# Optimization experiments

Hardware: AMD Instinct MI355X
Metric: run time of the kernel (lower is better)

## Reference

```python
import jax, jax.numpy as jnp
import numpy as np

B, K, S, H = 8, 2048, 1024, 256   # batch, num_spans, seq_len, hidden
W = 24                            # max span width (gather window)
WIN = 3
NEG_INF = -jnp.inf


def setup_inputs() -> dict:
    key = jax.random.key(0)
    k1, k2, k3, k4 = jax.random.split(key, 4)
    token_reps = jax.random.normal(k1, (B, S, H), dtype=jnp.float32)
    starts = jax.random.randint(k2, (B, K), 0, S - W)
    widths = jax.random.randint(k3, (B, K), 1, W + 1)  # span width in [1, W]
    ends = starts + widths                              # end is exclusive, <= S
    span_ids = jnp.stack([starts, ends], axis=-1).astype(jnp.int32)
    span_masks = jax.random.uniform(k4, (B, K)) < 0.9
    return {"token_reps": token_reps, "span_ids": span_ids, "span_masks": span_masks}


def _masked_max(tok_win, mask):
    # tok_win: (B, K, W, H), mask: (B, K, W) -> (B, K, H)
    return jnp.max(jnp.where(mask[..., None], tok_win, NEG_INF), axis=2)


def reference(token_reps, span_ids, span_masks):
    """extract_span_reps, mode='start_inner_maxpool_end', pooling=False.

    Equivalent math to the torch version, but gathers only the per-span window
    [start, start+W) instead of broadcasting over the full seq_len, since all
    spans have width <= W.
    """
    Bv, Sv, Hv = token_reps.shape
    starts = span_ids[..., 0]            # (B, K)
    ends = span_ids[..., 1]              # (B, K) exclusive

    pos = jnp.arange(W)                  # (W,)
    idx = starts[..., None] + pos        # (B, K, W) absolute token index
    safe_idx = jnp.clip(idx, 0, Sv - 1)  # safe gather; out-of-span masked below
    # gather per-span token windows: (B, K, W, H)
    tok_win = token_reps[jnp.arange(Bv)[:, None, None], safe_idx]

    valid = span_masks[..., None]                                 # (B, K, 1)
    start_cut = jnp.minimum(starts + WIN, ends)[..., None]        # (B, K, 1)
    end_cut = jnp.maximum(ends - WIN, starts)[..., None]          # (B, K, 1)
    e = ends[..., None]

    # idx >= start always holds (pos >= 0)
    start_m = (idx < start_cut) & valid
    end_m = (idx >= end_cut) & (idx < e) & valid
    inner_m = ((idx >= start_cut) & (idx < end_cut)
               & ((ends - starts) > 2 * WIN)[..., None] & valid)

    start_reps = _masked_max(tok_win, start_m)   # (B, K, H)
    end_reps = _masked_max(tok_win, end_m)
    inner_reps = _masked_max(tok_win, inner_m)

    # spans with no inner tokens fall back to start reps
    no_inner = jnp.isinf(inner_reps).all(axis=-1, keepdims=True)
    inner_reps = jnp.where(no_inner, start_reps, inner_reps)

    span_reps = jnp.concatenate([start_reps, inner_reps, end_reps], axis=-1)
    span_reps = jnp.where(span_masks[..., None], span_reps, 0.0)  # (B, K, 3H)
    return span_reps
```

## Files before the change

kernel.cpp:

```cpp
#include <hip/hip_runtime.h>

#define Bv   8
#define Kv   2048
#define Sv   1024
#define Hv   256
#define Wv   24
#define WINv 3
#define RB   8

#define NSPAN (Bv * Kv)

__device__ __forceinline__ float bf16_to_f32(unsigned short u) {
    union { unsigned int i; float f; } c;
    c.i = ((unsigned int)u) << 16;
    return c.f;
}

__global__ __launch_bounds__(256) void span_rep_kernel(
    const void* __restrict__ token_reps,
    const int* __restrict__ span_ids,
    const void* __restrict__ span_masks,
    float* __restrict__ out)
{
    __shared__ int s_tok32;
    __shared__ int s_ids64;
    __shared__ int s_maskw;

    const int tid = threadIdx.x;
    if (tid < 64) {
        const unsigned short* tu = (const unsigned short*)token_reps;
        int e = (tu[2 * tid] >> 7) & 0xFF;
        unsigned long long votes = __ballot(e >= 96 && e <= 144);

        const unsigned char* mb = (const unsigned char*)span_masks;
        unsigned char bnz = mb[tid] | mb[tid + 64];
        int m4 = tid & 3;
        unsigned long long z1  = __ballot(bnz && m4 == 1);
        unsigned long long z23 = __ballot(bnz && (m4 == 2 || m4 == 3));
        unsigned long long z84 = __ballot(bnz && m4 == 0 && (tid & 7) == 4);

        if (tid == 0) {
            s_tok32 = (__popcll(votes) >= 56) ? 0 : 1;
            s_maskw = z1 ? 0 : (z23 ? 3 : (z84 ? 1 : 2));
            int odd_or = span_ids[1] | span_ids[3] | span_ids[5] | span_ids[7];
            s_ids64 = (odd_or == 0) ? 1 : 0;
        }
    }
    __syncthreads();

    const int span = blockIdx.x * 4 + (tid >> 6);
    const int lane = tid & 63;

    float4* out4 = (float4*)(out + (size_t)span * (3 * Hv)) + lane;

    int mv;
    if (s_maskw == 0)      mv = ((const unsigned char*)span_masks)[span];
    else if (s_maskw == 1) mv = ((const int*)span_masks)[span];
    else if (s_maskw == 2) mv = ((const int*)span_masks)[2 * span];
    else                   mv = (((const float*)span_masks)[span] != 0.0f);

    int start, end;
    if (!s_ids64) {
        start = span_ids[2 * span];
        end   = span_ids[2 * span + 1];
    } else {
        start = span_ids[4 * span];
        end   = span_ids[4 * span + 2];
    }
    const int w = end - start;

    if (mv == 0 || w < 1 || w > Wv || start < 0 || end > Sv) {
        float4 z = make_float4(0.f, 0.f, 0.f, 0.f);
        out4[0]       = z;
        out4[Hv / 4]  = z;
        out4[Hv / 2]  = z;
        return;
    }

    const int b = span >> 11;
    const size_t row0 = ((size_t)b * Sv + start) * Hv;

    float s0 = -INFINITY, s1 = -INFINITY, s2 = -INFINITY, s3 = -INFINITY;
    float e0 = -INFINITY, e1 = -INFINITY, e2 = -INFINITY, e3 = -INFINITY;
    float i0 = -INFINITY, i1 = -INFINITY, i2 = -INFINITY, i3 = -INFINITY;

    const int  scut      = (w < WINv) ? w : WINv;
    const int  ecut      = (w - WINv > 0) ? (w - WINv) : 0;
    const bool has_inner = (w > 2 * WINv);
    const int  icut      = w - WINv;

    if (s_tok32) {
        const float4* tp = (const float4*)((const float*)token_reps + row0) + lane;
        for (int r0 = 0; r0 < w; r0 += RB) {
            const int n = ((w - r0) < RB) ? (w - r0) : RB;
            float4 buf[RB];
            #pragma unroll
            for (int j = 0; j < RB; ++j)
                if (j < n) buf[j] = tp[(size_t)(r0 + j) * (Hv / 4)];
            #pragma unroll
            for (int j = 0; j < RB; ++j) {
                if (j < n) {
                    const int r = r0 + j;
                    float4 f = buf[j];
                    if (r < scut) {
                        s0 = fmaxf(s0, f.x); s1 = fmaxf(s1, f.y);
                        s2 = fmaxf(s2, f.z); s3 = fmaxf(s3, f.w);
                    }
                    if (r >= ecut) {
                        e0 = fmaxf(e0, f.x); e1 = fmaxf(e1, f.y);
                        e2 = fmaxf(e2, f.z); e3 = fmaxf(e3, f.w);
                    }
                    if (has_inner && r >= WINv && r < icut) {
                        i0 = fmaxf(i0, f.x); i1 = fmaxf(i1, f.y);
                        i2 = fmaxf(i2, f.z); i3 = fmaxf(i3, f.w);
                    }
                }
            }
        }
    } else {
        const unsigned short* tp = (const unsigned short*)token_reps + row0 + lane * 4;
        for (int r0 = 0; r0 < w; r0 += RB) {
            const int n = ((w - r0) < RB) ? (w - r0) : RB;
            ushort4 buf[RB];
            #pragma unroll
            for (int j = 0; j < RB; ++j)
                if (j < n) buf[j] = *(const ushort4*)(tp + (size_t)(r0 + j) * Hv);
            #pragma unroll
            for (int j = 0; j < RB; ++j) {
                if (j < n) {
                    const int r = r0 + j;
                    float f0 = bf16_to_f32(buf[j].x), f1 = bf16_to_f32(buf[j].y);
                    float f2 = bf16_to_f32(buf[j].z), f3 = bf16_to_f32(buf[j].w);
                    if (r < scut) {
                        s0 = fmaxf(s0, f0); s1 = fmaxf(s1, f1);
                        s2 = fmaxf(s2, f2); s3 = fmaxf(s3, f3);
                    }
                    if (r >= ecut) {
                        e0 = fmaxf(e0, f0); e1 = fmaxf(e1, f1);
                        e2 = fmaxf(e2, f2); e3 = fmaxf(e3, f3);
                    }
                    if (has_inner && r >= WINv && r < icut) {
                        i0 = fmaxf(i0, f0); i1 = fmaxf(i1, f1);
                        i2 = fmaxf(i2, f2); i3 = fmaxf(i3, f3);
                    }
                }
            }
        }
    }
    if (!has_inner) { i0 = s0; i1 = s1; i2 = s2; i3 = s3; }

    out4[0]      = make_float4(s0, s1, s2, s3);
    out4[Hv / 4] = make_float4(i0, i1, i2, i3);
    out4[Hv / 2] = make_float4(e0, e1, e2, e3);
}

extern "C" void kernel_launch(void* const* d_in, const int* in_sizes, int n_in,
                              void* d_out, int out_size, void* d_ws, size_t ws_size,
                              hipStream_t stream) {
    const void* token_reps = d_in[0];
    const int*  span_ids   = (const int*)d_in[1];
    const void* span_masks = d_in[2];
    for (int i = 0; i < n_in; ++i) {
        if (in_sizes[i] == Bv * Sv * Hv)      token_reps = d_in[i];
        else if (in_sizes[i] == Bv * Kv * 2)  span_ids   = (const int*)d_in[i];
        else if (in_sizes[i] == Bv * Kv)      span_masks = d_in[i];
    }
    float* out = (float*)d_out;

    dim3 grid(NSPAN / 4);
    dim3 block(256);
    span_rep_kernel<<<grid, block, 0, stream>>>(token_reps, span_ids, span_masks, out);
}
```

Baseline: 91.00 us.

## Process eight spans per wave, drop shared-memory format probe, use nontemporal stores

Each wavefront now handles eight consecutive spans instead of one, and the grid shrinks to match. Blocks are interleaved across batches, so concurrently running blocks read from different batch rows. The per-block input-format detection moves from a shared-memory write followed by a barrier to per-wave ballots, which removes the __syncthreads. Outputs are written with nontemporal stores so they do not pollute the cache. In exchange, far fewer waves are in flight to hide gather latency, and every wave repeats the format probe loads.

Result: slower. 97.44 us (+7.1%).

```diff
diff --git a/kernel.cpp b/kernel.cpp
--- a/kernel.cpp
+++ b/kernel.cpp
@@ -7,13 +7,21 @@
 #define Wv   24
 #define WINv 3
 #define RB   8
+#define SPW  8
 
 #define NSPAN (Bv * Kv)
+
+typedef float nt4 __attribute__((ext_vector_type(4)));
 
 __device__ __forceinline__ float bf16_to_f32(unsigned short u) {
     union { unsigned int i; float f; } c;
     c.i = ((unsigned int)u) << 16;
     return c.f;
+}
+
+__device__ __forceinline__ void nt_store4(float* p, float a, float b, float c, float d) {
+    nt4 v = {a, b, c, d};
+    __builtin_nontemporal_store(v, (nt4*)p);
 }
 
 __global__ __launch_bounds__(256) void span_rep_kernel(
@@ -22,136 +30,123 @@
     const void* __restrict__ span_masks,
     float* __restrict__ out)
 {
-    __shared__ int s_tok32;
-    __shared__ int s_ids64;
-    __shared__ int s_maskw;
-
-    const int tid = threadIdx.x;
-    if (tid < 64) {
-        const unsigned short* tu = (const unsigned short*)token_reps;
-        int e = (tu[2 * tid] >> 7) & 0xFF;
-        unsigned long long votes = __ballot(e >= 96 && e <= 144);
-
-        const unsigned char* mb = (const unsigned char*)span_masks;
-        unsigned char bnz = mb[tid] | mb[tid + 64];
-        int m4 = tid & 3;
-        unsigned long long z1  = __ballot(bnz && m4 == 1);
-        unsigned long long z23 = __ballot(bnz && (m4 == 2 || m4 == 3));
-        unsigned long long z84 = __ballot(bnz && m4 == 0 && (tid & 7) == 4);
-
-        if (tid == 0) {
-            s_tok32 = (__popcll(votes) >= 56) ? 0 : 1;
-            s_maskw = z1 ? 0 : (z23 ? 3 : (z84 ? 1 : 2));
-            int odd_or = span_ids[1] | span_ids[3] | span_ids[5] | span_ids[7];
-            s_ids64 = (odd_or == 0) ? 1 : 0;
-        }
-    }
-    __syncthreads();
-
-    const int span = blockIdx.x * 4 + (tid >> 6);
+    const int tid  = threadIdx.x;
     const int lane = tid & 63;
 
-    float4* out4 = (float4*)(out + (size_t)span * (3 * Hv)) + lane;
+    const unsigned short* tu = (const unsigned short*)token_reps;
+    int e = (tu[2 * lane] >> 7) & 0xFF;
+    unsigned long long votes = __ballot(e >= 96 && e <= 144);
+    const int tok32 = (__popcll(votes) >= 56) ? 0 : 1;
 
-    int mv;
-    if (s_maskw == 0)      mv = ((const unsigned char*)span_masks)[span];
-    else if (s_maskw == 1) mv = ((const int*)span_masks)[span];
-    else if (s_maskw == 2) mv = ((const int*)span_masks)[2 * span];
-    else                   mv = (((const float*)span_masks)[span] != 0.0f);
+    const unsigned char* mbp = (const unsigned char*)span_masks;
+    unsigned char bnz = mbp[lane] | mbp[lane + 64];
+    int m4 = lane & 3;
+    unsigned long long z1  = __ballot(bnz && m4 == 1);
+    unsigned long long z23 = __ballot(bnz && (m4 == 2 || m4 == 3));
+    unsigned long long z84 = __ballot(bnz && m4 == 0 && (lane & 7) == 4);
+    const int maskw = z1 ? 0 : (z23 ? 3 : (z84 ? 1 : 2));
 
-    int start, end;
-    if (!s_ids64) {
-        start = span_ids[2 * span];
-        end   = span_ids[2 * span + 1];
-    } else {
-        start = span_ids[4 * span];
-        end   = span_ids[4 * span + 2];
-    }
-    const int w = end - start;
+    const int odd_or = span_ids[1] | span_ids[3] | span_ids[5] | span_ids[7];
+    const int ids64 = (odd_or == 0) ? 1 : 0;
 
-    if (mv == 0 || w < 1 || w > Wv || start < 0 || end > Sv) {
-        float4 z = make_float4(0.f, 0.f, 0.f, 0.f);
-        out4[0]       = z;
-        out4[Hv / 4]  = z;
-        out4[Hv / 2]  = z;
-        return;
+    const int b     = blockIdx.x & 7;
+    const int kbase = ((blockIdx.x >> 3) << 5) + ((tid >> 6) << 3);
+    const int span0 = b * Kv + kbase;
+
+    int st[SPW], en[SPW], mvv[SPW];
+    #pragma unroll
+    for (int j = 0; j < SPW; ++j) {
+        const int span = span0 + j;
+        if (!ids64) {
+            st[j] = span_ids[2 * span];
+            en[j] = span_ids[2 * span + 1];
+        } else {
+            st[j] = span_ids[4 * span];
+            en[j] = span_ids[4 * span + 2];
+        }
+        if (maskw == 0)      mvv[j] = ((const unsigned char*)span_masks)[span];
+        else if (maskw == 1) mvv[j] = ((const int*)span_masks)[span];
+        else if (maskw == 2) mvv[j] = ((const int*)span_masks)[2 * span];
+        else                 mvv[j] = (((const float*)span_masks)[span] != 0.0f);
     }
 
-    const int b = span >> 11;
-    const size_t row0 = ((size_t)b * Sv + start) * Hv;
+    const size_t batch_off = (size_t)b * Sv * Hv;
 
-    float s0 = -INFINITY, s1 = -INFINITY, s2 = -INFINITY, s3 = -INFINITY;
-    float e0 = -INFINITY, e1 = -INFINITY, e2 = -INFINITY, e3 = -INFINITY;
-    float i0 = -INFINITY, i1 = -INFINITY, i2 = -INFINITY, i3 = -INFINITY;
+    for (int j = 0; j < SPW; ++j) {
+        const int span = span0 + j;
+        float* outp = out + (size_t)span * (3 * Hv) + lane * 4;
 
-    const int  scut      = (w < WINv) ? w : WINv;
-    const int  ecut      = (w - WINv > 0) ? (w - WINv) : 0;
-    const bool has_inner = (w > 2 * WINv);
-    const int  icut      = w - WINv;
+        const int start = st[j];
+        const int w     = en[j] - start;
 
-    if (s_tok32) {
-        const float4* tp = (const float4*)((const float*)token_reps + row0) + lane;
-        for (int r0 = 0; r0 < w; r0 += RB) {
-            const int n = ((w - r0) < RB) ? (w - r0) : RB;
-            float4 buf[RB];
-            #pragma unroll
-            for (int j = 0; j < RB; ++j)
-                if (j < n) buf[j] = tp[(size_t)(r0 + j) * (Hv / 4)];
-            #pragma unroll
-            for (int j = 0; j < RB; ++j) {
-                if (j < n) {
-                    const int r = r0 + j;
-                    float4 f = buf[j];
-                    if (r < scut) {
-                        s0 = fmaxf(s0, f.x); s1 = fmaxf(s1, f.y);
-                        s2 = fmaxf(s2, f.z); s3 = fmaxf(s3, f.w);
-                    }
-                    if (r >= ecut) {
-                        e0 = fmaxf(e0, f.x); e1 = fmaxf(e1, f.y);
-                        e2 = fmaxf(e2, f.z); e3 = fmaxf(e3, f.w);
-                    }
-                    if (has_inner && r >= WINv && r < icut) {
-                        i0 = fmaxf(i0, f.x); i1 = fmaxf(i1, f.y);
-                        i2 = fmaxf(i2, f.z); i3 = fmaxf(i3, f.w);
-                    }
-                }
+        if (mvv[j] == 0 || w < 1 || w > Wv || start < 0 || en[j] > Sv) {
+            nt_store4(outp,          0.f, 0.f, 0.f, 0.f);
+            nt_store4(outp + Hv,     0.f, 0.f, 0.f, 0.f);
+            nt_store4(outp + 2 * Hv, 0.f, 0.f, 0.f, 0.f);
+            continue;
+        }
+
+        const size_t row0 = batch_off + (size_t)start * Hv;
+
+        float s0 = -INFINITY, s1 = -INFINITY, s2 = -INFINITY, s3 = -INFINITY;
+        float e0 = -INFINITY, e1 = -INFINITY, e2 = -INFINITY, e3 = -INFINITY;
+        float i0 = -INFINITY, i1 = -INFINITY, i2 = -INFINITY, i3 = -INFINITY;
+
+        const int  scut      = (w < WINv) ? w : WINv;
+        const int  ecut      = (w - WINv > 0) ? (w - WINv) : 0;
+        const bool has_inner = (w > 2 * WINv);
+        const int  icut      = w - WINv;
+
+        auto reduce = [&](int r, float f0, float f1, float f2, float f3) {
+            if (r < scut) {
+                s0 = fmaxf(s0, f0); s1 = fmaxf(s1, f1);
+                s2 = fmaxf(s2, f2); s3 = fmaxf(s3, f3);
+            }
+            if (r >= ecut) {
+                e0 = fmaxf(e0, f0); e1 = fmaxf(e1, f1);
+                e2 = fmaxf(e2, f2); e3 = fmaxf(e3, f3);
+            }
+            if (has_inner && r >= WINv && r < icut) {
+                i0 = fmaxf(i0, f0); i1 = fmaxf(i1, f1);
+                i2 = fmaxf(i2, f2); i3 = fmaxf(i3, f3);
+            }
+        };
+
+        if (tok32) {
+            const float4* tp = (const float4*)((const float*)token_reps + row0) + lane;
+            for (int r0 = 0; r0 < w; r0 += RB) {
+                const int n = ((w - r0) < RB) ? (w - r0) : RB;
+                float4 buf[RB];
+                #pragma unroll
+                for (int jj = 0; jj < RB; ++jj)
+                    if (jj < n) buf[jj] = tp[(size_t)(r0 + jj) * (Hv / 4)];
+                #pragma unroll
+                for (int jj = 0; jj < RB; ++jj)
+                    if (jj < n)
+                        reduce(r0 + jj, buf[jj].x, buf[jj].y, buf[jj].z, buf[jj].w);
+            }
+        } else {
+            const unsigned short* tp = (const unsigned short*)token_reps + row0 + lane * 4;
+            for (int r0 = 0; r0 < w; r0 += RB) {
+                const int n = ((w - r0) < RB) ? (w - r0) : RB;
+                ushort4 buf[RB];
+                #pragma unroll
+                for (int jj = 0; jj < RB; ++jj)
+                    if (jj < n) buf[jj] = *(const ushort4*)(tp + (size_t)(r0 + jj) * Hv);
+                #pragma unroll
+                for (int jj = 0; jj < RB; ++jj)
+                    if (jj < n)
+                        reduce(r0 + jj,
+                               bf16_to_f32(buf[jj].x), bf16_to_f32(buf[jj].y),
+                               bf16_to_f32(buf[jj].z), bf16_to_f32(buf[jj].w));
             }
         }
-    } else {
-        const unsigned short* tp = (const unsigned short*)token_reps + row0 + lane * 4;
-        for (int r0 = 0; r0 < w; r0 += RB) {
-            const int n = ((w - r0) < RB) ? (w - r0) : RB;
-            ushort4 buf[RB];
-            #pragma unroll
-            for (int j = 0; j < RB; ++j)
-                if (j < n) buf[j] = *(const ushort4*)(tp + (size_t)(r0 + j) * Hv);
-            #pragma unroll
-            for (int j = 0; j < RB; ++j) {
-                if (j < n) {
-                    const int r = r0 + j;
-                    float f0 = bf16_to_f32(buf[j].x), f1 = bf16_to_f32(buf[j].y);
-                    float f2 = bf16_to_f32(buf[j].z), f3 = bf16_to_f32(buf[j].w);
-                    if (r < scut) {
-                        s0 = fmaxf(s0, f0); s1 = fmaxf(s1, f1);
-                        s2 = fmaxf(s2, f2); s3 = fmaxf(s3, f3);
-                    }
-                    if (r >= ecut) {
-                        e0 = fmaxf(e0, f0); e1 = fmaxf(e1, f1);
-                        e2 = fmaxf(e2, f2); e3 = fmaxf(e3, f3);
-                    }
-                    if (has_inner && r >= WINv && r < icut) {
-                        i0 = fmaxf(i0, f0); i1 = fmaxf(i1, f1);
-                        i2 = fmaxf(i2, f2); i3 = fmaxf(i3, f3);
-                    }
-                }
-            }
-        }
+        if (!has_inner) { i0 = s0; i1 = s1; i2 = s2; i3 = s3; }
+
+        nt_store4(outp,          s0, s1, s2, s3);
+        nt_store4(outp + Hv,     i0, i1, i2, i3);
+        nt_store4(outp + 2 * Hv, e0, e1, e2, e3);
     }
-    if (!has_inner) { i0 = s0; i1 = s1; i2 = s2; i3 = s3; }
-
-    out4[0]      = make_float4(s0, s1, s2, s3);
-    out4[Hv / 4] = make_float4(i0, i1, i2, i3);
-    out4[Hv / 2] = make_float4(e0, e1, e2, e3);
 }
 
 extern "C" void kernel_launch(void* const* d_in, const int* in_sizes, int n_in,
@@ -167,7 +162,7 @@
     }
     float* out = (float*)d_out;
 
-    dim3 grid(NSPAN / 4);
+    dim3 grid(NSPAN / (4 * SPW));
     dim3 block(256);
     span_rep_kernel<<<grid, block, 0, stream>>>(token_reps, span_ids, span_masks, out);
 }
```
